# Performance work log

Hardware: AMD Instinct MI355X
Metric: run time of the kernel (lower is better)

Reference implementation:

```python
import jax, jax.numpy as jnp
import numpy as np

N = 50000      # nodes
E = 400000     # edges (before self loops)
IN = 128       # in_channels
H = 4          # num_heads (layers 1-2)
C = 32         # hidden_dim per head
HID = H * C    # 128 total hidden
CLS = 40       # num_classes (out_heads = 1)
EPS = 1e-5     # BatchNorm eps
SLOPE = 0.2    # LeakyReLU negative slope (PyG GATConv default)


def setup_inputs() -> dict:
    key = jax.random.key(0)
    ks = jax.random.split(key, 24)
    rn = lambda k, shp, s: jax.random.normal(k, shp, jnp.float32) * s
    x = jax.random.normal(ks[0], (N, IN), jnp.float32)
    src = jax.random.randint(ks[1], (E,), 0, N)
    dst = jax.random.randint(ks[2], (E,), 0, N)
    src = jnp.where(src == dst, (src + 1) % N, src)  # no pre-existing self loops
    edge_index = jnp.stack([src, dst]).astype(jnp.int32)
    inp = dict(x=x, edge_index=edge_index)
    # conv1: in IN -> H heads x C
    inp['W1'] = rn(ks[3], (IN, H * C), 1.0 / np.sqrt(IN))
    inp['as1'] = rn(ks[4], (H, C), 0.1)
    inp['ad1'] = rn(ks[5], (H, C), 0.1)
    inp['b1'] = rn(ks[6], (H * C,), 0.02)
    # conv2: HID -> H x C
    inp['W2'] = rn(ks[7], (HID, H * C), 1.0 / np.sqrt(HID))
    inp['as2'] = rn(ks[8], (H, C), 0.1)
    inp['ad2'] = rn(ks[9], (H, C), 0.1)
    inp['b2'] = rn(ks[10], (H * C,), 0.02)
    # conv3: HID -> 1 head x CLS, concat=False
    inp['W3'] = rn(ks[11], (HID, CLS), 1.0 / np.sqrt(HID))
    inp['as3'] = rn(ks[12], (1, CLS), 0.1)
    inp['ad3'] = rn(ks[13], (1, CLS), 0.1)
    inp['b3'] = rn(ks[14], (CLS,), 0.02)
    # residual projection
    inp['Wres'] = rn(ks[15], (IN, HID), 1.0 / np.sqrt(IN))
    # BatchNorm (eval mode: running stats)
    inp['g1'] = 1.0 + rn(ks[16], (HID,), 0.1)
    inp['be1'] = rn(ks[17], (HID,), 0.1)
    inp['m1'] = rn(ks[18], (HID,), 0.1)
    inp['v1'] = 1.0 + jax.random.uniform(ks[19], (HID,), jnp.float32) * 0.5
    inp['g2'] = 1.0 + rn(ks[20], (HID,), 0.1)
    inp['be2'] = rn(ks[21], (HID,), 0.1)
    inp['m2'] = rn(ks[22], (HID,), 0.1)
    inp['v2'] = 1.0 + jax.random.uniform(ks[23], (HID,), jnp.float32) * 0.5
    return inp


def _gat_conv(h, src, dst, W, a_src, a_dst, bias, heads, out_ch, concat):
    """PyG-style GATConv (eval: attention dropout off), self loops already in src/dst."""
    n = h.shape[0]
    xw = (h @ W).reshape(n, heads, out_ch)                    # [N,H,C]
    e_src = jnp.sum(xw * a_src, axis=-1)                      # [N,H]
    e_dst = jnp.sum(xw * a_dst, axis=-1)                      # [N,H]
    e = jax.nn.leaky_relu(e_src[src] + e_dst[dst], SLOPE)     # [E',H]
    # segment softmax over incoming edges of each dst node
    mseg = jax.ops.segment_max(e, dst, num_segments=n)        # [N,H]
    ex = jnp.exp(e - mseg[dst])
    den = jax.ops.segment_sum(ex, dst, num_segments=n)
    alpha = ex / den[dst]                                     # [E',H]
    out = jax.ops.segment_sum(alpha[:, :, None] * xw[src], dst, num_segments=n)  # [N,H,C]
    out = out.reshape(n, heads * out_ch) if concat else out.mean(axis=1)
    return out + bias


def _bn(h, g, b, m, v):
    return (h - m) * jax.lax.rsqrt(v + EPS) * g + b


def reference(x, edge_index, W1, as1, ad1, b1, W2, as2, ad2, b2,
              W3, as3, ad3, b3, Wres, g1, be1, m1, v1, g2, be2, m2, v2):
    n = x.shape[0]
    loop = jnp.arange(n, dtype=edge_index.dtype)
    src = jnp.concatenate([edge_index[0], loop])  # add self loops (PyG default)
    dst = jnp.concatenate([edge_index[1], loop])
    x0 = x
    h = _gat_conv(x0, src, dst, W1, as1, ad1, b1, H, C, True)
    h = jax.nn.elu(_bn(h, g1, be1, m1, v1) + x0 @ Wres)
    h_res = h
    h = _gat_conv(h, src, dst, W2, as2, ad2, b2, H, C, True)
    h = jax.nn.elu(_bn(h, g2, be2, m2, v2) + h_res)
    logits = _gat_conv(h, src, dst, W3, as3, ad3, b3, 1, CLS, False)
    return logits
```

## Files before the change

kernel.cpp:

```cpp
#include <hip/hip_runtime.h>
#include <hip/hip_bf16.h>

#define THREADS 256

typedef __attribute__((ext_vector_type(8))) short bfrag;
typedef __attribute__((ext_vector_type(4))) float f32x4;

__device__ inline unsigned short f2b(float v) {
    __hip_bfloat16 b = __float2bfloat16(v);
    return *reinterpret_cast<unsigned short*>(&b);
}
__device__ inline float b2f(unsigned short u) {
    return __uint_as_float(((unsigned)u) << 16);
}
__device__ inline float rdv(const void* p, int off, bool isbf) {
    return isbf ? b2f(((const unsigned short*)p)[off]) : ((const float*)p)[off];
}

struct InPtrs { const void* p[23]; };

__global__ void prep_kernel(InPtrs in, int* __restrict__ flag,
                            unsigned short* __restrict__ Wl1, unsigned short* __restrict__ Wl2,
                            unsigned short* __restrict__ WlR, unsigned short* __restrict__ Wl3,
                            float* __restrict__ bnsc1, float* __restrict__ bnsh1,
                            float* __restrict__ bnsc2, float* __restrict__ bnsh2,
                            float* __restrict__ B3f,
                            int N, const int* __restrict__ ei, int* __restrict__ deg,
                            int E) {
    int b = blockIdx.x, tid = threadIdx.x;
    if (b >= 30) {
        int i = (b - 30) * 256 + tid;
        if (i < E + N) {
            int d = (i < E) ? ei[E + i] : (i - E);
            atomicAdd(&deg[d], 1);
        }
        return;
    }
    __shared__ int sred[4];
    const unsigned short* x = (const unsigned short*)in.p[0];
    int local = 0;
    for (int i = tid; i < 4096; i += 256) {
        unsigned ex = (x[i] >> 7) & 0xFF;
        if (ex == 0xFF || ex >= 134 || (ex > 0 && ex <= 100)) local++;
    }
#pragma unroll
    for (int o = 1; o < 64; o <<= 1) local += __shfl_xor(local, o, 64);
    if ((tid & 63) == 0) sred[tid >> 6] = local;
    __syncthreads();
    bool isbf = !((sred[0] + sred[1] + sred[2] + sred[3]) * 8 > 4096);

    if (b < 29) {
        const void *Wv, *asp = 0, *adp = 0; unsigned short* o; int cols, C = 0, FH = 0, tt;
        if (b < 9)       { Wv = in.p[2];  asp = in.p[3];  adp = in.p[4];  o = Wl1; cols = 128; C = 32; FH = 4; tt = b; }
        else if (b < 18) { Wv = in.p[6];  asp = in.p[7];  adp = in.p[8];  o = Wl2; cols = 128; C = 32; FH = 4; tt = b - 9; }
        else if (b < 26) { Wv = in.p[14];                                 o = WlR; cols = 128;                 tt = b - 18; }
        else             { Wv = in.p[10]; asp = in.p[11]; adp = in.p[12]; o = Wl3; cols = 40;  C = 40; FH = 1; tt = b - 26; }
        int id = tt * 256 + tid;
        int ks = (id >> 6) & 3, l = id & 63;
        int q = l >> 4, n = l & 15;
        int c = tt * 16 + n;
#pragma unroll
        for (int j = 0; j < 8; ++j) {
            int k = ks * 32 + q * 8 + j;
            float v = 0.f;
            if (c < cols) {
                v = rdv(Wv, k * cols + c, isbf);
            } else if (FH && c < cols + 2 * FH) {
                int dn = c - cols;
                int h = dn < FH ? dn : dn - FH;
                const void* av = dn < FH ? asp : adp;
                float s = 0.f;
                for (int cc = 0; cc < C; ++cc)
                    s += rdv(Wv, k * cols + h * C + cc, isbf) * rdv(av, h * C + cc, isbf);
                v = s;
            }
            o[id * 8 + j] = f2b(v);
        }
    } else {
        int c = tid;
        if (c < 128) {
            float s = rdv(in.p[15], c, isbf) * rsqrtf(rdv(in.p[18], c, isbf) + 1e-5f);
            bnsc1[c] = s;
            bnsh1[c] = rdv(in.p[16], c, isbf) - rdv(in.p[17], c, isbf) * s +
                       rdv(in.p[5], c, isbf) * s;
        } else {
            int d = c - 128;
            float s = rdv(in.p[19], d, isbf) * rsqrtf(rdv(in.p[22], d, isbf) + 1e-5f);
            bnsc2[d] = s;
            bnsh2[d] = rdv(in.p[20], d, isbf) - rdv(in.p[21], d, isbf) * s +
                       rdv(in.p[9], d, isbf) * s;
            if (d < 40) B3f[d] = rdv(in.p[13], d, isbf);
        }
        if (tid == 0) *flag = isbf ? 1 : 0;
    }
}

__global__ __launch_bounds__(256) void scan_kernel(
    const int* __restrict__ deg, unsigned long long* __restrict__ look,
    int* __restrict__ row_ptr, int* __restrict__ pos, int N) {
    int b = blockIdx.x, tid = threadIdx.x;
    int lane = tid & 63, wv = tid >> 6;
    __shared__ int ws[4];
    __shared__ int s_off;
    int idx = b * 256 + tid;
    int v = (idx < N) ? deg[idx] : 0;
    int sc = v;
#pragma unroll
    for (int o = 1; o < 64; o <<= 1) {
        int t = __shfl_up(sc, o, 64);
        if (lane >= o) sc += t;
    }
    if (lane == 63) ws[wv] = sc;
    __syncthreads();
    int tot = ws[0] + ws[1] + ws[2] + ws[3];
    if (tid == 0)
        atomicExch(&look[b], (1ULL << 32) | (unsigned)tot);
    if (wv == 0) {
        int run = 0;
        if (b > 0) {
            int base = b - 1;
            for (;;) {
                int i = base - lane;
                unsigned long long st = (i >= 0) ? atomicAdd(&look[i], 0ULL)
                                                 : (2ULL << 32);
                int status = (int)(st >> 32);
                int val = (int)(st & 0xffffffffULL);
                unsigned long long bp = __ballot(status == 2);
                unsigned long long bz = __ballot(status == 0);
                int fp = bp ? (__ffsll(bp) - 1) : 64;
                int fz = bz ? (__ffsll(bz) - 1) : 64;
                if (fz < fp) continue;
                int contrib = (lane <= fp) ? val : 0;
#pragma unroll
                for (int o = 1; o < 64; o <<= 1) contrib += __shfl_xor(contrib, o, 64);
                run += contrib;
                if (fp < 64) break;
                base -= 64;
            }
        }
        if (lane == 0) {
            s_off = run;
            atomicExch(&look[b], (2ULL << 32) | (unsigned)(run + tot));
        }
    }
    __syncthreads();
    int add = s_off;
#pragma unroll
    for (int k = 0; k < 4; ++k) add += (k < wv) ? ws[k] : 0;
    int excl = add + sc - v;
    if (idx < N) {
        pos[idx] = excl;
        row_ptr[idx + 1] = excl + v;
    }
    if (idx == 0) row_ptr[0] = 0;
}

__global__ void scatter_kernel(const int* __restrict__ ei, int* __restrict__ pos,
                               int* __restrict__ csr, int E, int N) {
    int e = blockIdx.x * THREADS + threadIdx.x;
    if (e >= E + N) return;
    int s, d;
    if (e < E) { s = ei[e]; d = ei[E + e]; }
    else { s = e - E; d = s; }
    int p = atomicAdd(&pos[d], 1);
    csr[p] = s;
}

template <int COLT, int HEADS, int ESCOL>
__global__ __launch_bounds__(256) void gemm_mfma(
    const unsigned short* __restrict__ A, const unsigned short* __restrict__ Wg,
    unsigned short* __restrict__ out, int ldc, int cols,
    float* __restrict__ es, float* __restrict__ ed, int N) {
    __shared__ __align__(16) unsigned short Wls[COLT * 2048];
    int tid = threadIdx.x;
    {
        const float4* src = (const float4*)Wg;
        float4* dst = (float4*)Wls;
#pragma unroll
        for (int i = 0; i < COLT; ++i) dst[tid + i * 256] = src[tid + i * 256];
    }
    __syncthreads();
    int w = tid >> 6, lane = tid & 63;
    int n = lane & 15, q = lane >> 4;
    int row0 = blockIdx.x * 64 + w * 16;
    int ar = row0 + n; ar = ar < N ? ar : N - 1;
    f32x4 acc[COLT];
#pragma unroll
    for (int t = 0; t < COLT; ++t) acc[t] = (f32x4){0.f, 0.f, 0.f, 0.f};
    const unsigned short* arow = A + (size_t)ar * 128;
#pragma unroll
    for (int ks = 0; ks < 4; ++ks) {
        bfrag a = *reinterpret_cast<const bfrag*>(arow + ks * 32 + q * 8);
#pragma unroll
        for (int t = 0; t < COLT; ++t) {
            bfrag b = *reinterpret_cast<const bfrag*>(&Wls[((t * 4 + ks) * 64 + lane) * 8]);
            acc[t] = __builtin_amdgcn_mfma_f32_16x16x32_bf16(a, b, acc[t], 0, 0, 0);
        }
    }
    constexpr int TE = ESCOL >> 4, NE = ESCOL & 15;
    int dn = n - NE;
#pragma unroll
    for (int r = 0; r < 4; ++r) {
        int row = row0 + q * 4 + r;
        if (row < N) {
            if (dn >= 0 && dn < HEADS) es[(size_t)row * HEADS + dn] = acc[TE][r];
            else if (dn >= HEADS && dn < 2 * HEADS)
                ed[(size_t)row * HEADS + (dn - HEADS)] = acc[TE][r];
        }
    }
#pragma unroll
    for (int t = 0; t < COLT; ++t) {
        int col = t * 16 + n;
        if (col < cols) {
#pragma unroll
            for (int r = 0; r < 4; ++r) {
                int row = row0 + q * 4 + r;
                if (row < N) out[(size_t)row * ldc + col] = f2b(acc[t][r]);
            }
        }
    }
}

__global__ __launch_bounds__(256) void gemm_dual(
    const void* __restrict__ Ain, const int* __restrict__ flag,
    const unsigned short* __restrict__ Wg1, const unsigned short* __restrict__ WgR,
    unsigned short* __restrict__ xwb, unsigned short* __restrict__ resb,
    float* __restrict__ es, float* __restrict__ ed, int N) {
    __shared__ __align__(16) unsigned short Wls[16 * 2048];
    int tid = threadIdx.x;
    {
        const float4* s1 = (const float4*)Wg1;
        const float4* s2 = (const float4*)WgR;
        float4* dst = (float4*)Wls;
#pragma unroll
        for (int i = 0; i < 8; ++i) dst[tid + i * 256] = s1[tid + i * 256];
#pragma unroll
        for (int i = 0; i < 8; ++i) dst[2048 + tid + i * 256] = s2[tid + i * 256];
    }
    bool isbf = (*flag != 0);
    __syncthreads();
    int w = tid >> 6, lane = tid & 63;
    int n = lane & 15, q = lane >> 4;
    int row0 = blockIdx.x * 64 + w * 16;
    int ar = row0 + n; ar = ar < N ? ar : N - 1;
    bfrag a[4];
    if (isbf) {
        const unsigned short* arow = (const unsigned short*)Ain + (size_t)ar * 128;
#pragma unroll
        for (int ks = 0; ks < 4; ++ks)
            a[ks] = *reinterpret_cast<const bfrag*>(arow + ks * 32 + q * 8);
    } else {
        const float* arow = (const float*)Ain + (size_t)ar * 128;
#pragma unroll
        for (int ks = 0; ks < 4; ++ks) {
            float4 f0 = *reinterpret_cast<const float4*>(arow + ks * 32 + q * 8);
            float4 f1 = *reinterpret_cast<const float4*>(arow + ks * 32 + q * 8 + 4);
            bfrag t;
            t[0] = (short)f2b(f0.x); t[1] = (short)f2b(f0.y);
            t[2] = (short)f2b(f0.z); t[3] = (short)f2b(f0.w);
            t[4] = (short)f2b(f1.x); t[5] = (short)f2b(f1.y);
            t[6] = (short)f2b(f1.z); t[7] = (short)f2b(f1.w);
            a[ks] = t;
        }
    }
    f32x4 acc[16], accE;
#pragma unroll
    for (int t = 0; t < 16; ++t) acc[t] = (f32x4){0.f, 0.f, 0.f, 0.f};
    accE = (f32x4){0.f, 0.f, 0.f, 0.f};
#pragma unroll
    for (int ks = 0; ks < 4; ++ks) {
#pragma unroll
        for (int t = 0; t < 8; ++t) {
            bfrag b = *reinterpret_cast<const bfrag*>(&Wls[((t * 4 + ks) * 64 + lane) * 8]);
            acc[t] = __builtin_amdgcn_mfma_f32_16x16x32_bf16(a[ks], b, acc[t], 0, 0, 0);
        }
        bfrag be = *reinterpret_cast<const bfrag*>(Wg1 + ((size_t)(32 + ks) * 64 + lane) * 8);
        accE = __builtin_amdgcn_mfma_f32_16x16x32_bf16(a[ks], be, accE, 0, 0, 0);
#pragma unroll
        for (int t = 0; t < 8; ++t) {
            bfrag b = *reinterpret_cast<const bfrag*>(&Wls[16384 + ((t * 4 + ks) * 64 + lane) * 8]);
            acc[8 + t] = __builtin_amdgcn_mfma_f32_16x16x32_bf16(a[ks], b, acc[8 + t], 0, 0, 0);
        }
    }
#pragma unroll
    for (int r = 0; r < 4; ++r) {
        int row = row0 + q * 4 + r;
        if (row < N) {
            if (n < 4) es[(size_t)row * 4 + n] = accE[r];
            else if (n < 8) ed[(size_t)row * 4 + (n - 4)] = accE[r];
        }
    }
#pragma unroll
    for (int t = 0; t < 8; ++t) {
        int col = t * 16 + n;
#pragma unroll
        for (int r = 0; r < 4; ++r) {
            int row = row0 + q * 4 + r;
            if (row < N) {
                xwb[(size_t)row * 128 + col] = f2b(acc[t][r]);
                resb[(size_t)row * 128 + col] = f2b(acc[8 + t][r]);
            }
        }
    }
}

__global__ __launch_bounds__(256) void agg128_fused(
    const unsigned short* __restrict__ xwb, const float* __restrict__ es,
    const float* __restrict__ ed, const int* __restrict__ row_ptr,
    const int* __restrict__ csr, const float* __restrict__ bnsc,
    const float* __restrict__ bnsh, const unsigned short* __restrict__ resb,
    unsigned short* __restrict__ outb, int N) {
    int w = threadIdx.x >> 6, lane = threadIdx.x & 63;
    int node = blockIdx.x * 4 + w;
    if (node >= N) return;
    int h = lane >> 4;
    int c0 = lane * 2;
    float edl = ed[node * 4 + h];
    int start = __builtin_amdgcn_readfirstlane(row_ptr[node]);
    int end = __builtin_amdgcn_readfirstlane(row_ptr[node + 1]);
    float den = 0.f, a0 = 0.f, a1 = 0.f;
    for (int jb = start; jb < end; jb += 16) {
        int su[16];
#pragma unroll
        for (int u = 0; u < 16; ++u) {
            int idx = jb + u;
            idx = idx < end - 1 ? idx : end - 1;
            su[u] = csr[idx];
        }
        unsigned uu[16];
        float ev[16];
#pragma unroll
        for (int u = 0; u < 16; ++u) {
            uu[u] = *(const unsigned*)(xwb + (size_t)su[u] * 128 + c0);
            ev[u] = es[su[u] * 4 + h];
        }
#pragma unroll
        for (int u = 0; u < 16; ++u) {
            float e = ev[u] + edl;
            e = e > 0.f ? e : 0.2f * e;
            float wg = __expf(e);
            wg = (jb + u < end) ? wg : 0.f;
            den += wg;
            a0 = fmaf(wg, __uint_as_float(uu[u] << 16), a0);
            a1 = fmaf(wg, __uint_as_float(uu[u] & 0xffff0000u), a1);
        }
    }
    float inv = 1.f / den;
    float2 sc = *(const float2*)(bnsc + c0);
    float2 sh = *(const float2*)(bnsh + c0);
    unsigned ur = *(const unsigned*)(resb + (size_t)node * 128 + c0);
    float v0 = fmaf(a0 * inv, sc.x, sh.x) + __uint_as_float(ur << 16);
    float v1 = fmaf(a1 * inv, sc.y, sh.y) + __uint_as_float(ur & 0xffff0000u);
    v0 = v0 > 0.f ? v0 : expm1f(v0);
    v1 = v1 > 0.f ? v1 : expm1f(v1);
    unsigned pk = (unsigned)f2b(v0) | ((unsigned)f2b(v1) << 16);
    *(unsigned*)(outb + (size_t)node * 128 + c0) = pk;
}

__global__ __launch_bounds__(256) void agg40_kernel(
    const unsigned short* __restrict__ xw3b, const float* __restrict__ es3,
    const float* __restrict__ ed3, const int* __restrict__ row_ptr,
    const int* __restrict__ csr, const float* __restrict__ b3,
    void* __restrict__ out, const int* __restrict__ flag, int N) {
    int w = threadIdx.x >> 6, lane = threadIdx.x & 63;
    int node = blockIdx.x * 4 + w;
    if (node >= N) return;
    int i16 = lane & 15;
    int g = lane >= 40 ? 2 : (lane >= 20 ? 1 : 0);
    int cp = lane - g * 20;
    int c0 = cp * 2; c0 = c0 > 38 ? 38 : c0;
    float edl = ed3[node];
    int start = row_ptr[node], end = row_ptr[node + 1];
    float den = 0.f, a0 = 0.f, a1 = 0.f;
    for (int jb = start; jb < end; jb += 16) {
        int cnt = end - jb; cnt = cnt < 16 ? cnt : 16;
        int sv = csr[jb + (i16 < cnt ? i16 : 0)];
        unsigned uu[6];
#pragma unroll
        for (int t = 0; t < 6; ++t) {
            int slot = 3 * t + g; slot = slot < 15 ? slot : 15;
            int s = __shfl(sv, slot, 64);
            uu[t] = *(const unsigned*)(xw3b + (size_t)s * 40 + c0);
        }
        float wgl = 0.f;
        if (i16 < cnt) {
            float e = es3[sv] + edl;
            e = e > 0.f ? e : 0.2f * e;
            wgl = __expf(e);
        }
        float d = wgl;
        d += __shfl_xor(d, 1, 64);
        d += __shfl_xor(d, 2, 64);
        d += __shfl_xor(d, 4, 64);
        d += __shfl_xor(d, 8, 64);
        den += d;
#pragma unroll
        for (int t = 0; t < 6; ++t) {
            int slot = 3 * t + g;
            int sl = slot < 15 ? slot : 15;
            float wg = __shfl(wgl, sl, 64);
            if (slot >= cnt) wg = 0.f;
            a0 = fmaf(wg, __uint_as_float(uu[t] << 16), a0);
            a1 = fmaf(wg, __uint_as_float(uu[t] & 0xffff0000u), a1);
        }
    }
    float t0 = __shfl(a0, (lane + 20) & 63, 64);
    float t1 = __shfl(a0, (lane + 40) & 63, 64);
    float u0 = __shfl(a1, (lane + 20) & 63, 64);
    float u1 = __shfl(a1, (lane + 40) & 63, 64);
    a0 += t0 + t1;
    a1 += u0 + u1;
    if (lane < 20) {
        float inv = 1.f / den;
        float v0 = a0 * inv + b3[c0];
        float v1 = a1 * inv + b3[c0 + 1];
        size_t eoff = (size_t)node * 40 + c0;
        if (*flag) {
            unsigned pk = (unsigned)f2b(v0) | ((unsigned)f2b(v1) << 16);
            *(unsigned*)((unsigned short*)out + eoff) = pk;
        } else {
            *(float2*)((float*)out + eoff) = make_float2(v0, v1);
        }
    }
}

extern "C" void kernel_launch(void* const* d_in, const int* in_sizes, int n_in,
                              void* d_out, int out_size, void* d_ws, size_t ws_size,
                              hipStream_t stream) {
    (void)n_in; (void)out_size; (void)ws_size;
    const int N = in_sizes[0] / 128;
    const int E = in_sizes[1] / 2;
    const int EPN = E + N;
    const int NB = (N + 255) / 256;
    const int CB = (EPN + 255) / 256;
    char* base = (char*)d_ws;
    size_t off = 0;
    auto alloc = [&](size_t bytes) -> char* {
        char* p = base + off;
        off = (off + bytes + 255) & ~(size_t)255;
        return p;
    };
    int* flag = (int*)alloc(4);
    size_t degB = ((size_t)N * 4 + 7) & ~(size_t)7;
    char* zreg = alloc(degB + (size_t)NB * 8);
    int* deg = (int*)zreg;
    unsigned long long* look = (unsigned long long*)(zreg + degB);
    int* row_ptr = (int*)alloc((size_t)(N + 1) * 4);
    int* pos = (int*)alloc((size_t)N * 4);
    int* csr = (int*)alloc((size_t)EPN * 4);
    float* bnsc1 = (float*)alloc(512); float* bnsh1 = (float*)alloc(512);
    float* bnsc2 = (float*)alloc(512); float* bnsh2 = (float*)alloc(512);
    float* B3f = (float*)alloc(256);
    unsigned short* Wl1 = (unsigned short*)alloc(36864);
    unsigned short* Wl2 = (unsigned short*)alloc(36864);
    unsigned short* WlR = (unsigned short*)alloc(32768);
    unsigned short* Wl3 = (unsigned short*)alloc(12288);
    unsigned short* xwb = (unsigned short*)alloc((size_t)N * 128 * 2);
    unsigned short* h1b = (unsigned short*)alloc((size_t)N * 128 * 2);
    unsigned short* resb = (unsigned short*)alloc((size_t)N * 128 * 2);
    float* es = (float*)alloc((size_t)N * 4 * 4);
    float* ed = (float*)alloc((size_t)N * 4 * 4);

    const int* ei = (const int*)d_in[1];

    hipMemsetAsync(zreg, 0, degB + (size_t)NB * 8, stream);

    InPtrs ip;
    for (int t = 0; t < 23; t++) ip.p[t] = d_in[t];
    prep_kernel<<<30 + CB, THREADS, 0, stream>>>(ip, flag, Wl1, Wl2, WlR, Wl3,
                                                 bnsc1, bnsh1, bnsc2, bnsh2,
                                                 B3f, N, ei, deg, E);

    scan_kernel<<<NB, 256, 0, stream>>>(deg, look, row_ptr, pos, N);
    scatter_kernel<<<(EPN + THREADS - 1) / THREADS, THREADS, 0, stream>>>(ei, pos, csr, E, N);

    int gemmGrid = (N + 63) / 64;
    int aggGrid = (N + 3) / 4;

    gemm_dual<<<gemmGrid, 256, 0, stream>>>(d_in[0], flag, Wl1, WlR,
                                            xwb, resb, es, ed, N);
    agg128_fused<<<aggGrid, 256, 0, stream>>>(xwb, es, ed, row_ptr, csr,
                                              bnsc1, bnsh1, resb, h1b, N);
    gemm_mfma<9, 4, 128><<<gemmGrid, 256, 0, stream>>>(
        h1b, Wl2, xwb, 128, 128, es, ed, N);
    unsigned short* h2b = resb;
    agg128_fused<<<aggGrid, 256, 0, stream>>>(xwb, es, ed, row_ptr, csr,
                                              bnsc2, bnsh2, h1b, h2b, N);
    gemm_mfma<3, 1, 40><<<gemmGrid, 256, 0, stream>>>(
        h2b, Wl3, xwb, 40, 40, es, ed, N);
    agg40_kernel<<<aggGrid, 256, 0, stream>>>(xwb, es, ed, row_ptr, csr, B3f,
                                              d_out, flag, N);
}
```

Measured before the change: 314.4 us.

## Split degree counters into 8 slices and replace lookback scan with three-pass scan

Degree counting and CSR scatter now use eight per-slice counter arrays, chosen by edge index, to spread atomic contention. The decoupled-lookback scan becomes a reduce, single-block scan and downsweep that writes a separate position per slice. Each slice gets an ordered CSR segment, which keeps neighbour order more deterministic. The cost is eight times more counter memory, a larger memset and two extra kernel launches.

```diff
diff --git a/kernel.cpp b/kernel.cpp
--- a/kernel.cpp
+++ b/kernel.cpp
@@ -25,14 +25,15 @@
                             float* __restrict__ bnsc1, float* __restrict__ bnsh1,
                             float* __restrict__ bnsc2, float* __restrict__ bnsh2,
                             float* __restrict__ B3f,
-                            int N, const int* __restrict__ ei, int* __restrict__ deg,
-                            int E) {
+                            int N, const int* __restrict__ ei, int* __restrict__ deg8,
+                            int E, int DB) {
     int b = blockIdx.x, tid = threadIdx.x;
     if (b >= 30) {
-        int i = (b - 30) * 256 + tid;
-        if (i < E + N) {
+        int stride = DB * 256;
+        for (int i = (b - 30) * 256 + tid; i < E + N; i += stride) {
             int d = (i < E) ? ei[E + i] : (i - E);
-            atomicAdd(&deg[d], 1);
+            int k = (i >> 10) & 7;
+            atomicAdd(&deg8[k * N + d], 1);
         }
         return;
     }
@@ -95,15 +96,27 @@
     }
 }
 
-__global__ __launch_bounds__(256) void scan_kernel(
-    const int* __restrict__ deg, unsigned long long* __restrict__ look,
-    int* __restrict__ row_ptr, int* __restrict__ pos, int N) {
-    int b = blockIdx.x, tid = threadIdx.x;
-    int lane = tid & 63, wv = tid >> 6;
+__global__ void bsum_kernel(const int* __restrict__ deg8, int* __restrict__ bsum, int N) {
+    int idx = blockIdx.x * 256 + threadIdx.x;
+    int lane = threadIdx.x & 63, wv = threadIdx.x >> 6;
+    int v = 0;
+    if (idx < N) {
+#pragma unroll
+        for (int k = 0; k < 8; ++k) v += deg8[k * N + idx];
+    }
+#pragma unroll
+    for (int o = 1; o < 64; o <<= 1) v += __shfl_xor(v, o, 64);
     __shared__ int ws[4];
-    __shared__ int s_off;
-    int idx = b * 256 + tid;
-    int v = (idx < N) ? deg[idx] : 0;
+    if (lane == 0) ws[wv] = v;
+    __syncthreads();
+    if (threadIdx.x == 0) bsum[blockIdx.x] = ws[0] + ws[1] + ws[2] + ws[3];
+}
+
+__global__ __launch_bounds__(1024) void bscan_kernel(const int* __restrict__ bsum,
+                                                     int* __restrict__ boff, int nb) {
+    __shared__ int ws[16];
+    int tid = threadIdx.x, lane = tid & 63, wv = tid >> 6;
+    int v = (tid < nb) ? bsum[tid] : 0;
     int sc = v;
 #pragma unroll
     for (int o = 1; o < 64; o <<= 1) {
@@ -112,58 +125,58 @@
     }
     if (lane == 63) ws[wv] = sc;
     __syncthreads();
-    int tot = ws[0] + ws[1] + ws[2] + ws[3];
-    if (tid == 0)
-        atomicExch(&look[b], (1ULL << 32) | (unsigned)tot);
-    if (wv == 0) {
-        int run = 0;
-        if (b > 0) {
-            int base = b - 1;
-            for (;;) {
-                int i = base - lane;
-                unsigned long long st = (i >= 0) ? atomicAdd(&look[i], 0ULL)
-                                                 : (2ULL << 32);
-                int status = (int)(st >> 32);
-                int val = (int)(st & 0xffffffffULL);
-                unsigned long long bp = __ballot(status == 2);
-                unsigned long long bz = __ballot(status == 0);
-                int fp = bp ? (__ffsll(bp) - 1) : 64;
-                int fz = bz ? (__ffsll(bz) - 1) : 64;
-                if (fz < fp) continue;
-                int contrib = (lane <= fp) ? val : 0;
-#pragma unroll
-                for (int o = 1; o < 64; o <<= 1) contrib += __shfl_xor(contrib, o, 64);
-                run += contrib;
-                if (fp < 64) break;
-                base -= 64;
-            }
-        }
-        if (lane == 0) {
-            s_off = run;
-            atomicExch(&look[b], (2ULL << 32) | (unsigned)(run + tot));
-        }
-    }
+    int add = 0;
+#pragma unroll
+    for (int k = 0; k < 16; ++k) add += (k < wv) ? ws[k] : 0;
+    if (tid < nb) boff[tid] = add + sc - v;
+}
+
+__global__ void scanw_kernel(const int* __restrict__ deg8, const int* __restrict__ boff,
+                             int* __restrict__ row_ptr, int* __restrict__ posk, int N) {
+    int idx = blockIdx.x * 256 + threadIdx.x;
+    int lane = threadIdx.x & 63, wv = threadIdx.x >> 6;
+    int vk[8];
+    int v = 0;
+    if (idx < N) {
+#pragma unroll
+        for (int k = 0; k < 8; ++k) { vk[k] = deg8[k * N + idx]; v += vk[k]; }
+    } else {
+#pragma unroll
+        for (int k = 0; k < 8; ++k) vk[k] = 0;
+    }
+    int sc = v;
+#pragma unroll
+    for (int o = 1; o < 64; o <<= 1) {
+        int t = __shfl_up(sc, o, 64);
+        if (lane >= o) sc += t;
+    }
+    __shared__ int ws[4];
+    if (lane == 63) ws[wv] = sc;
     __syncthreads();
-    int add = s_off;
+    int add = boff[blockIdx.x];
 #pragma unroll
     for (int k = 0; k < 4; ++k) add += (k < wv) ? ws[k] : 0;
     int excl = add + sc - v;
     if (idx < N) {
-        pos[idx] = excl;
         row_ptr[idx + 1] = excl + v;
+        int run = excl;
+#pragma unroll
+        for (int k = 0; k < 8; ++k) { posk[k * N + idx] = run; run += vk[k]; }
     }
     if (idx == 0) row_ptr[0] = 0;
 }
 
-__global__ void scatter_kernel(const int* __restrict__ ei, int* __restrict__ pos,
-                               int* __restrict__ csr, int E, int N) {
-    int e = blockIdx.x * THREADS + threadIdx.x;
-    if (e >= E + N) return;
-    int s, d;
-    if (e < E) { s = ei[e]; d = ei[E + e]; }
-    else { s = e - E; d = s; }
-    int p = atomicAdd(&pos[d], 1);
-    csr[p] = s;
+__global__ void scatter_kernel(const int* __restrict__ ei, int* __restrict__ posk,
+                               int* __restrict__ csr, int E, int N, int DB) {
+    int stride = DB * 256;
+    for (int i = blockIdx.x * 256 + threadIdx.x; i < E + N; i += stride) {
+        int s, d;
+        if (i < E) { s = ei[i]; d = ei[E + i]; }
+        else { s = i - E; d = s; }
+        int k = (i >> 10) & 7;
+        int p = atomicAdd(&posk[k * N + d], 1);
+        csr[p] = s;
+    }
 }
 
 template <int COLT, int HEADS, int ESCOL>
@@ -432,7 +445,7 @@
     const int E = in_sizes[1] / 2;
     const int EPN = E + N;
     const int NB = (N + 255) / 256;
-    const int CB = (EPN + 255) / 256;
+    const int DB = (EPN + 1023) / 1024;
     char* base = (char*)d_ws;
     size_t off = 0;
     auto alloc = [&](size_t bytes) -> char* {
@@ -441,12 +454,11 @@
         return p;
     };
     int* flag = (int*)alloc(4);
-    size_t degB = ((size_t)N * 4 + 7) & ~(size_t)7;
-    char* zreg = alloc(degB + (size_t)NB * 8);
-    int* deg = (int*)zreg;
-    unsigned long long* look = (unsigned long long*)(zreg + degB);
+    int* deg8 = (int*)alloc((size_t)N * 8 * 4);
+    int* posk = (int*)alloc((size_t)N * 8 * 4);
     int* row_ptr = (int*)alloc((size_t)(N + 1) * 4);
-    int* pos = (int*)alloc((size_t)N * 4);
+    int* bsum = (int*)alloc((size_t)NB * 4);
+    int* boff = (int*)alloc((size_t)NB * 4);
     int* csr = (int*)alloc((size_t)EPN * 4);
     float* bnsc1 = (float*)alloc(512); float* bnsh1 = (float*)alloc(512);
     float* bnsc2 = (float*)alloc(512); float* bnsh2 = (float*)alloc(512);
@@ -463,16 +475,18 @@
 
     const int* ei = (const int*)d_in[1];
 
-    hipMemsetAsync(zreg, 0, degB + (size_t)NB * 8, stream);
+    hipMemsetAsync(deg8, 0, (size_t)N * 8 * 4, stream);
 
     InPtrs ip;
     for (int t = 0; t < 23; t++) ip.p[t] = d_in[t];
-    prep_kernel<<<30 + CB, THREADS, 0, stream>>>(ip, flag, Wl1, Wl2, WlR, Wl3,
+    prep_kernel<<<30 + DB, THREADS, 0, stream>>>(ip, flag, Wl1, Wl2, WlR, Wl3,
                                                  bnsc1, bnsh1, bnsc2, bnsh2,
-                                                 B3f, N, ei, deg, E);
-
-    scan_kernel<<<NB, 256, 0, stream>>>(deg, look, row_ptr, pos, N);
-    scatter_kernel<<<(EPN + THREADS - 1) / THREADS, THREADS, 0, stream>>>(ei, pos, csr, E, N);
+                                                 B3f, N, ei, deg8, E, DB);
+
+    bsum_kernel<<<NB, 256, 0, stream>>>(deg8, bsum, N);
+    bscan_kernel<<<1, 1024, 0, stream>>>(bsum, boff, NB);
+    scanw_kernel<<<NB, 256, 0, stream>>>(deg8, boff, row_ptr, posk, N);
+    scatter_kernel<<<DB, 256, 0, stream>>>(ei, posk, csr, E, N, DB);
 
     int gemmGrid = (N + 63) / 64;
     int aggGrid = (N + 3) / 4;
```

Result: faster. 304.5 us (-3.2%).
